# Kernel tuning notes

Measured on AMD Instinct MI355X. Metric: run time of the kernel, lower is better.

## Reference

```python
import jax, jax.numpy as jnp
import numpy as np

B, L, HID = 2, 2048, 2048
N_HEAD, HEAD_DIM, N_KV = 32, 64, 8
N_Q_PER_KV = N_HEAD // N_KV  # 4
SCALE = 0.125  # 1/sqrt(HEAD_DIM)
PAD_START = L - 256  # last 256 key positions are padding
NEG = -1e9


def setup_inputs() -> dict:
    key = jax.random.key(0)
    ks = jax.random.split(key, 8)
    query = jax.random.normal(ks[0], (B, L, HID), jnp.float32)
    kv = jax.random.normal(ks[1], (B, L, HID), jnp.float32)
    # additive causal mask (0 on/below diagonal, -1e9 above)
    i = jnp.arange(L)
    attn_mask = jnp.where(i[None, :] > i[:, None], NEG, 0.0).astype(jnp.float32)
    # key padding mask: True == padded position
    key_padding_mask = (i[None, :] >= PAD_START) & jnp.ones((B, 1), bool)
    s = 0.02
    Wq = jax.random.normal(ks[2], (HID, N_HEAD * HEAD_DIM), jnp.float32) * s
    bq = jnp.zeros((N_HEAD * HEAD_DIM,), jnp.float32)
    Wkv = jax.random.normal(ks[3], (HID, 2 * N_KV * HEAD_DIM), jnp.float32) * s
    bkv = jnp.zeros((2 * N_KV * HEAD_DIM,), jnp.float32)
    Wo = jax.random.normal(ks[4], (N_HEAD * HEAD_DIM, HID), jnp.float32) * s
    bo = jnp.zeros((HID,), jnp.float32)
    return {"query": query, "kv": kv, "Wq": Wq, "bq": bq, "Wkv": Wkv,
            "bkv": bkv, "Wo": Wo, "bo": bo, "attn_mask": attn_mask,
            "key_padding_mask": key_padding_mask}


def reference(query, kv, Wq, bq, Wkv, bkv, Wo, bo, attn_mask, key_padding_mask):
    b, l, _ = query.shape
    q = (query @ Wq + bq).reshape(b, l, N_HEAD, HEAD_DIM).transpose(0, 2, 1, 3)  # [B,H,L,D]
    kvp = kv @ Wkv + bkv                                   # [B,L,2*NKV*D]
    k, v = jnp.split(kvp, 2, axis=-1)
    k = k.reshape(b, l, N_KV, HEAD_DIM)
    v = v.reshape(b, l, N_KV, HEAD_DIM)
    # GQA: repeat_interleave KV heads to match Q heads
    k = jnp.repeat(k, N_Q_PER_KV, axis=2).transpose(0, 2, 1, 3)  # [B,H,L,D]
    v = jnp.repeat(v, N_Q_PER_KV, axis=2).transpose(0, 2, 1, 3)
    qk = jnp.einsum('bhqd,bhkd->bhqk', q, k) * SCALE
    qk = qk + attn_mask                                     # additive mask
    qk = jnp.where(key_padding_mask[:, None, None, :], NEG, qk)
    p = jax.nn.softmax(qk.astype(jnp.float32), axis=-1).astype(q.dtype)
    attn = jnp.einsum('bhqk,bhkd->bhqd', p, v)
    attn = attn.transpose(0, 2, 1, 3).reshape(b, l, N_HEAD * HEAD_DIM)
    out = attn @ Wo + bo
    return out
```

## Files before the change

kernel.cpp:

```cpp
#include <hip/hip_runtime.h>
#include <stdint.h>

#define L_SEQ 2048
#define HID 2048
#define PADK 1792
#define QSCALE 0.18033688011112042f

typedef unsigned short us_t;
typedef __attribute__((ext_vector_type(8))) short bf16x8;
typedef __attribute__((ext_vector_type(4))) float f32x4;

__device__ __forceinline__ float bf2f(us_t u) {
    union { unsigned int i; float f; } c; c.i = ((unsigned int)u) << 16; return c.f;
}
__device__ __forceinline__ us_t f2bf(float f) {
    union { float f; unsigned int i; } c; c.f = f;
    unsigned int i = c.i;
    return (us_t)((i + 0x7FFFu + ((i >> 16) & 1u)) >> 16);
}
__device__ __forceinline__ unsigned int pk_bf16(float a, float b) {
#if __has_builtin(__builtin_amdgcn_cvt_pk_bf16_f32)
    auto r = __builtin_amdgcn_cvt_pk_bf16_f32(a, b);
    unsigned int u; __builtin_memcpy(&u, &r, 4); return u;
#else
    return (unsigned int)f2bf(a) | ((unsigned int)f2bf(b) << 16);
#endif
}
__device__ __forceinline__ float fast_exp2(float x) {
#if __has_builtin(__builtin_amdgcn_exp2f)
    return __builtin_amdgcn_exp2f(x);
#else
    return exp2f(x);
#endif
}
__device__ __forceinline__ void gload_lds16(const us_t* g, us_t* l) {
    __builtin_amdgcn_global_load_lds((const __attribute__((address_space(1))) void*)g,
                                     (__attribute__((address_space(3))) void*)l, 16, 0, 0);
}
__device__ __forceinline__ int detect_bf16(const unsigned int* q) {
    __shared__ int sc[4];
    unsigned int v = q[threadIdx.x & 255];
    unsigned int e = (v >> 7) & 0xFFu;
    unsigned long long bb = __ballot(e >= 112u && e <= 133u);
    int cnt = __popcll(bb);
    if ((threadIdx.x & 63) == 0) sc[threadIdx.x >> 6] = cnt;
    __syncthreads();
    return (sc[0] + sc[1] + sc[2] + sc[3]) > 128;
}
__device__ __forceinline__ int detect_bf16_512(const unsigned int* q) {
    __shared__ int sc[8];
    unsigned int v = q[threadIdx.x & 255];
    unsigned int e = (v >> 7) & 0xFFu;
    unsigned long long bb = __ballot(e >= 112u && e <= 133u);
    int cnt = __popcll(bb);
    if ((threadIdx.x & 63) == 0) sc[threadIdx.x >> 6] = cnt;
    __syncthreads();
    int s = 0;
    #pragma unroll
    for (int i = 0; i < 8; ++i) s += sc[i];
    return s > 256;
}

__global__ __launch_bounds__(256) void prep(const unsigned int* __restrict__ qdet,
                                            const void* __restrict__ query,
                                            const void* __restrict__ kvsrc,
                                            const void* __restrict__ Wq,
                                            const void* __restrict__ Wkv,
                                            const void* __restrict__ Wo,
                                            us_t* __restrict__ Aq, us_t* __restrict__ Akv,
                                            us_t* __restrict__ Wqt, us_t* __restrict__ Wkvt,
                                            us_t* __restrict__ Wot) {
    __shared__ us_t tile[4096];
    const int bf = detect_bf16(qdet);
    int id = blockIdx.x;
    if (id < 8192) {
        const void* s = (id < 4096) ? query : kvsrc;
        us_t* d       = (id < 4096) ? Aq : Akv;
        int cid = (id & 4095) * 256 + threadIdx.x;
        if (bf) {
            ((bf16x8*)d)[cid] = ((const bf16x8*)s)[cid];
        } else {
            const float* sp = (const float*)s + (size_t)cid * 8;
            f32x4 a = *(const f32x4*)sp, b2 = *(const f32x4*)(sp + 4);
            union { bf16x8 v; unsigned int dw[4]; } o;
            o.dw[0] = pk_bf16(a[0], a[1]);   o.dw[1] = pk_bf16(a[2], a[3]);
            o.dw[2] = pk_bf16(b2[0], b2[1]); o.dw[3] = pk_bf16(b2[2], b2[3]);
            ((bf16x8*)d)[cid] = o.v;
        }
        return;
    }
    id -= 8192;
    const void* s; us_t* d; int R, C, bx, by;
    if (id < 1024)      { s = Wq;  d = Wqt;  R = 2048; C = 2048; bx = id & 31; by = id >> 5; }
    else if (id < 1536) { id -= 1024; s = Wkv; d = Wkvt; R = 2048; C = 1024; bx = id & 15; by = id >> 4; }
    else                { id -= 1536; s = Wo;  d = Wot;  R = 2048; C = 2048; bx = id & 31; by = id >> 5; }
    const int c0 = bx * 64, r0 = by * 64;
    const int t = threadIdx.x;
    const int r  = t >> 2;
    const int cq = (t & 3) * 16;
    bf16x8 lo, hi;
    if (bf) {
        const us_t* sp = (const us_t*)s + (size_t)(r0 + r) * C + c0 + cq;
        lo = *(const bf16x8*)sp;
        hi = *(const bf16x8*)(sp + 8);
    } else {
        const float* sp = (const float*)s + (size_t)(r0 + r) * C + c0 + cq;
        f32x4 a0 = *(const f32x4*)sp,       a1 = *(const f32x4*)(sp + 4);
        f32x4 a2 = *(const f32x4*)(sp + 8), a3 = *(const f32x4*)(sp + 12);
        union { bf16x8 v; unsigned int dw[4]; } ul, uh;
        ul.dw[0] = pk_bf16(a0[0], a0[1]); ul.dw[1] = pk_bf16(a0[2], a0[3]);
        ul.dw[2] = pk_bf16(a1[0], a1[1]); ul.dw[3] = pk_bf16(a1[2], a1[3]);
        uh.dw[0] = pk_bf16(a2[0], a2[1]); uh.dw[1] = pk_bf16(a2[2], a2[3]);
        uh.dw[2] = pk_bf16(a3[0], a3[1]); uh.dw[3] = pk_bf16(a3[2], a3[3]);
        lo = ul.v; hi = uh.v;
    }
    {
        us_t* base = &tile[r * 64];
        int ch0 = (2 * (t & 3))     ^ (r & 7);
        int ch1 = (2 * (t & 3) + 1) ^ (r & 7);
        *(bf16x8*)(base + ch0 * 8) = lo;
        *(bf16x8*)(base + ch1 * 8) = hi;
    }
    __syncthreads();
    const int c2 = t >> 2;
    const int rq = (t & 3) * 16;
    union { bf16x8 v; us_t e[8]; } w0, w1;
    #pragma unroll
    for (int j = 0; j < 8; ++j) {
        int ra = rq + j, rb = rq + 8 + j;
        w0.e[j] = tile[ra * 64 + (((c2 >> 3) ^ (ra & 7)) * 8) + (c2 & 7)];
        w1.e[j] = tile[rb * 64 + (((c2 >> 3) ^ (rb & 7)) * 8) + (c2 & 7)];
    }
    us_t* dp = d + (size_t)(c0 + c2) * R + r0 + rq;
    *(bf16x8*)dp       = w0.v;
    *(bf16x8*)(dp + 8) = w1.v;
}

template<int MQ, typename STG, typename TAIL>
__device__ __forceinline__ void phase2(const us_t* Ab, const us_t* Bb,
                                       int wm, int wn, int l15, int cs0, int cs1,
                                       bf16x8 (&bv)[4][2], f32x4 (&acc)[8][4],
                                       STG&& stg, TAIL&& tail) {
    bf16x8 af[4][2];
    #pragma unroll
    for (int mt = 0; mt < 4; ++mt) {
        const us_t* p = &Ab[(wm * 128 + MQ * 64 + mt * 16 + l15) * 64];
        af[mt][0] = *(const bf16x8*)&p[cs0 * 8];
        af[mt][1] = *(const bf16x8*)&p[cs1 * 8];
    }
    if (MQ == 0) {
        #pragma unroll
        for (int nt = 0; nt < 4; ++nt) {
            const us_t* p = &Bb[(wn * 64 + nt * 16 + l15) * 64];
            bv[nt][0] = *(const bf16x8*)&p[cs0 * 8];
            bv[nt][1] = *(const bf16x8*)&p[cs1 * 8];
        }
    }
    stg();
    __builtin_amdgcn_s_barrier();
    asm volatile("s_waitcnt lgkmcnt(0)" ::: "memory");
    __builtin_amdgcn_sched_barrier(0);
    __builtin_amdgcn_s_setprio(1);
    #pragma unroll
    for (int ki = 0; ki < 2; ++ki)
        #pragma unroll
        for (int mt = 0; mt < 4; ++mt)
            #pragma unroll
            for (int nt = 0; nt < 4; ++nt)
                acc[MQ * 4 + mt][nt] = __builtin_amdgcn_mfma_f32_16x16x32_bf16(
                    af[mt][ki], bv[nt][ki], acc[MQ * 4 + mt][nt], 0, 0, 0);
    __builtin_amdgcn_s_setprio(0);
    tail();
    __builtin_amdgcn_s_barrier();
}

__device__ __forceinline__ void gemm256(const us_t* __restrict__ Ag,
                                        const us_t* __restrict__ Bg,
                                        int bm, int bn, us_t* sh,
                                        f32x4 (&acc)[8][4]) {
    us_t* As0 = sh;           us_t* As1 = sh + 16384;
    us_t* Bs0 = sh + 32768;   us_t* Bs1 = sh + 49152;
    const int t = threadIdx.x;
    const int w = t >> 6, lane = t & 63, l15 = lane & 15, quad = lane >> 4;
    const int wm = w >> 2, wn = w & 3;
    const int cs0 = quad ^ (l15 & 7);
    const int cs1 = (4 + quad) ^ (l15 & 7);

    int aoff[2][2], boff[2][2], adst[2][2], bdst[2][2];
    #pragma unroll
    for (int u = 0; u < 2; ++u)
        #pragma unroll
        for (int j = 0; j < 2; ++j) {
            int row0 = j * 128 + u * 64 + w * 8;
            int row  = row0 + (lane >> 3);
            int col  = ((lane & 7) ^ (row & 7)) * 8;
            aoff[u][j] = (bm + row) * 2048 + col;
            adst[u][j] = row0 * 64;
            int ci   = w * 2 + j;
            int rb0  = (ci >> 2) * 64 + u * 32 + (ci & 3) * 8;
            int rowb = rb0 + (lane >> 3);
            int colb = ((lane & 7) ^ (rowb & 7)) * 8;
            boff[u][j] = (bn + rowb) * 2048 + colb;
            bdst[u][j] = rb0 * 64;
        }

#define STAGE_A(U, KT, DST) do { \
        gload_lds16(Ag + (size_t)aoff[U][0] + (KT) * 64, (DST) + adst[U][0]); \
        gload_lds16(Ag + (size_t)aoff[U][1] + (KT) * 64, (DST) + adst[U][1]); } while (0)
#define STAGE_B(U, KT, DST) do { \
        gload_lds16(Bg + (size_t)boff[U][0] + (KT) * 64, (DST) + bdst[U][0]); \
        gload_lds16(Bg + (size_t)boff[U][1] + (KT) * 64, (DST) + bdst[U][1]); } while (0)

    #pragma unroll
    for (int i = 0; i < 8; ++i)
        #pragma unroll
        for (int j = 0; j < 4; ++j) acc[i][j] = (f32x4){0.f, 0.f, 0.f, 0.f};

    STAGE_A(0, 0, As0); STAGE_B(0, 0, Bs0);
    STAGE_A(1, 0, As0); STAGE_B(1, 0, Bs0);
    STAGE_A(0, 1, As1); STAGE_B(0, 1, Bs1); STAGE_B(1, 1, Bs1);
    asm volatile("s_waitcnt vmcnt(6)" ::: "memory");
    __builtin_amdgcn_s_barrier();

    bf16x8 bv[4][2];
    #pragma unroll 1
    for (int it = 0; it < 16; ++it) {
        const bool more = (it < 15);
        const int kb = 2 * it + 1;
        phase2<0>(As0, Bs0, wm, wn, l15, cs0, cs1, bv, acc,
                  [&] { STAGE_A(1, kb, As1); },
                  [&] { asm volatile("s_waitcnt vmcnt(8)" ::: "memory"); });
        phase2<1>(As0, Bs0, wm, wn, l15, cs0, cs1, bv, acc,
                  [&] { if (more) { STAGE_A(0, kb + 1, As0); STAGE_B(0, kb + 1, Bs0);
                                    STAGE_B(1, kb + 1, Bs0); } },
                  [&] { if (more) asm volatile("s_waitcnt vmcnt(8)" ::: "memory");
                        else      asm volatile("s_waitcnt vmcnt(2)" ::: "memory"); });
        phase2<0>(As1, Bs1, wm, wn, l15, cs0, cs1, bv, acc,
                  [&] { if (more) STAGE_A(1, kb + 1, As0); },
                  [&] { if (more) asm volatile("s_waitcnt vmcnt(8)" ::: "memory");
                        else      asm volatile("s_waitcnt vmcnt(0)" ::: "memory"); });
        phase2<1>(As1, Bs1, wm, wn, l15, cs0, cs1, bv, acc,
                  [&] { if (more) { STAGE_A(0, kb + 2, As1); STAGE_B(0, kb + 2, Bs1);
                                    STAGE_B(1, kb + 2, Bs1); } },
                  [&] { if (more) asm volatile("s_waitcnt vmcnt(8)" ::: "memory"); });
    }
#undef STAGE_A
#undef STAGE_B
}

__global__ __launch_bounds__(512, 2) void qkv_gemm(const unsigned int* __restrict__ qdet,
                                                   const us_t* __restrict__ Aq,
                                                   const us_t* __restrict__ Akv,
                                                   const us_t* __restrict__ Wqt,
                                                   const us_t* __restrict__ Wkvt,
                                                   const void* __restrict__ bq,
                                                   const void* __restrict__ bkv,
                                                   us_t* __restrict__ Qm,
                                                   us_t* __restrict__ Km,
                                                   us_t* __restrict__ Vg) {
    __shared__ us_t sh[65536];
    const int bf = detect_bf16_512(qdet);
    const int t = threadIdx.x;
    const int w = t >> 6, lane = t & 63, l15 = lane & 15, quad = lane >> 4;
    const int wm = w >> 2, wn = w & 3;

    int bid = blockIdx.x;
    int id = (bid & 7) * 24 + (bid >> 3);
    const us_t* Ag; const us_t* Bg; int bm, bn; bool isQ;
    if (id < 128) { isQ = true;  Ag = Aq;  Bg = Wqt;  bm = (id >> 3) * 256; bn = (id & 7) * 256; }
    else { id -= 128; isQ = false; Ag = Akv; Bg = Wkvt; bm = (id >> 2) * 256; bn = (id & 3) * 256; }

    f32x4 acc[8][4];
    gemm256(Ag, Bg, bm, bn, sh, acc);

    if (isQ) {
        #pragma unroll
        for (int an = 0; an < 4; ++an) {
            int col = bn + wn * 64 + an * 16 + l15;
            float bvv = bf ? bf2f(((const us_t*)bq)[col]) : ((const float*)bq)[col];
            #pragma unroll
            for (int am = 0; am < 8; ++am)
                #pragma unroll
                for (int r = 0; r < 4; ++r) {
                    int row = bm + wm * 128 + am * 16 + quad * 4 + r;
                    Qm[(size_t)row * 2048 + col] = f2bf((acc[am][an][r] + bvv) * QSCALE);
                }
        }
    } else if (bn < 512) {
        #pragma unroll
        for (int an = 0; an < 4; ++an) {
            int col = bn + wn * 64 + an * 16 + l15;
            float bvv = bf ? bf2f(((const us_t*)bkv)[col]) : ((const float*)bkv)[col];
            #pragma unroll
            for (int am = 0; am < 8; ++am)
                #pragma unroll
                for (int r = 0; r < 4; ++r) {
                    int row = bm + wm * 128 + am * 16 + quad * 4 + r;
                    Km[(size_t)row * 512 + col] = f2bf(acc[am][an][r] + bvv);
                }
        }
    } else {
        const int b2 = bm >> 11, tok0 = bm & 2047;
        #pragma unroll
        for (int half = 0; half < 2; ++half) {
            __syncthreads();
            if ((wn >> 1) == half) {
                #pragma unroll
                for (int an = 0; an < 4; ++an) {
                    int col = bn + wn * 64 + an * 16 + l15;
                    float bvv = bf ? bf2f(((const us_t*)bkv)[col]) : ((const float*)bkv)[col];
                    int cl = (wn & 1) * 64 + an * 16 + l15;
                    #pragma unroll
                    for (int am = 0; am < 8; ++am)
                        #pragma unroll
                        for (int r = 0; r < 4; ++r) {
                            int tok = wm * 128 + am * 16 + quad * 4 + r;
                            sh[cl * 258 + tok] = f2bf(acc[am][an][r] + bvv);
                        }
                }
            }
            __syncthreads();
            size_t vrow0 = (size_t)(b2 * 512 + (bn - 512) + half * 128);
            #pragma unroll
            for (int jj = 0; jj < 8; ++jj) {
                int idx = t + jj * 512;
                int c2 = idx >> 5, ch = idx & 31;
                bf16x8 vv = *(const bf16x8*)&sh[c2 * 258 + ch * 8];
                *(bf16x8*)(Vg + (vrow0 + c2) * (size_t)2048 + tok0 + ch * 8) = vv;
            }
        }
    }
}

__device__ __forceinline__ void gemm_core(const us_t* __restrict__ A,
                                          const us_t* __restrict__ Bt,
                                          int K, int bm, int bn, int t,
                                          us_t (&As)[2][8192], us_t (&Bs)[2][8192],
                                          f32x4 (&acc)[4][4]) {
    const int w = t >> 6, lane = t & 63, l15 = lane & 15, quad = lane >> 4;
    const int wm = (w & 1) * 64, wn = (w >> 1) * 64;
    int rA[4], cA[4];
    #pragma unroll
    for (int i = 0; i < 4; ++i) {
        int p = (w * 4 + i) * 64 + lane;
        int row = p >> 3, cs = p & 7;
        rA[i] = row; cA[i] = (cs ^ (row & 7)) * 8;
    }
    #pragma unroll
    for (int i = 0; i < 4; ++i) {
        gload_lds16(A  + (size_t)(bm + rA[i]) * K + cA[i], &As[0][(w * 4 + i) * 512]);
        gload_lds16(Bt + (size_t)(bn + rA[i]) * K + cA[i], &Bs[0][(w * 4 + i) * 512]);
    }
    int pb = 0;
    for (int k0 = 0; k0 < K; k0 += 64) {
        __syncthreads();
        if (k0 + 64 < K) {
            #pragma unroll
            for (int i = 0; i < 4; ++i) {
                gload_lds16(A  + (size_t)(bm + rA[i]) * K + k0 + 64 + cA[i], &As[pb ^ 1][(w * 4 + i) * 512]);
                gload_lds16(Bt + (size_t)(bn + rA[i]) * K + k0 + 64 + cA[i], &Bs[pb ^ 1][(w * 4 + i) * 512]);
            }
        }
        #pragma unroll
        for (int ki = 0; ki < 2; ++ki) {
            bf16x8 af[4], bfr[4];
            #pragma unroll
            for (int mt = 0; mt < 4; ++mt) {
                int row = wm + mt * 16 + l15;
                int cs  = (ki * 4 + quad) ^ (row & 7);
                af[mt] = *(const bf16x8*)&As[pb][row * 64 + cs * 8];
            }
            #pragma unroll
            for (int nt = 0; nt < 4; ++nt) {
                int row = wn + nt * 16 + l15;
                int cs  = (ki * 4 + quad) ^ (row & 7);
                bfr[nt] = *(const bf16x8*)&Bs[pb][row * 64 + cs * 8];
            }
            #pragma unroll
            for (int mt = 0; mt < 4; ++mt)
                #pragma unroll
                for (int nt = 0; nt < 4; ++nt)
                    acc[mt][nt] = __builtin_amdgcn_mfma_f32_16x16x32_bf16(af[mt], bfr[nt], acc[mt][nt], 0, 0, 0);
        }
        pb ^= 1;
    }
}

__global__ __launch_bounds__(256, 2) void o_gemm(const unsigned int* __restrict__ qdet,
                                                 const us_t* __restrict__ Ao,
                                                 const us_t* __restrict__ Wot,
                                                 const void* __restrict__ bo,
                                                 void* __restrict__ Out) {
    __shared__ us_t As[2][8192], Bs[2][8192];
    const int bf = detect_bf16(qdet);
    const int t = threadIdx.x;
    const int w = t >> 6, lane = t & 63, l15 = lane & 15, quad = lane >> 4;
    const int wm = (w & 1) * 64, wn = (w >> 1) * 64;
    const int bid = blockIdx.x;
    const int lid = (bid & 7) * 64 + (bid >> 3);
    const int bm = (lid >> 4) * 128, bn = (lid & 15) * 128;
    f32x4 acc[4][4];
    #pragma unroll
    for (int i = 0; i < 4; ++i)
        #pragma unroll
        for (int j = 0; j < 4; ++j) acc[i][j] = (f32x4){0.f, 0.f, 0.f, 0.f};
    gemm_core(Ao, Wot, 2048, bm, bn, t, As, Bs, acc);
    #pragma unroll
    for (int nt = 0; nt < 4; ++nt) {
        int col = bn + wn + nt * 16 + l15;
        float bvv = bf ? bf2f(((const us_t*)bo)[col]) : ((const float*)bo)[col];
        #pragma unroll
        for (int mt = 0; mt < 4; ++mt)
            #pragma unroll
            for (int r = 0; r < 4; ++r) {
                int row = bm + wm + mt * 16 + quad * 4 + r;
                float v = acc[mt][nt][r] + bvv;
                if (bf) ((us_t*)Out)[(size_t)row * 2048 + col] = f2bf(v);
                else    ((float*)Out)[(size_t)row * 2048 + col] = v;
            }
    }
}

__device__ __forceinline__ void qk_exp(const bf16x8 kb[2][4], const bf16x8 qf[2][2],
                                       int q0, int k0, int l15, int quad,
                                       bf16x8 pa[2][2]) {
    f32x4 sa[2][4];
    #pragma unroll
    for (int mt = 0; mt < 2; ++mt)
        #pragma unroll
        for (int nt = 0; nt < 4; ++nt) sa[mt][nt] = (f32x4){0.f, 0.f, 0.f, 0.f};
    __builtin_amdgcn_s_setprio(1);
    #pragma unroll
    for (int ki = 0; ki < 2; ++ki)
        #pragma unroll
        for (int mt = 0; mt < 2; ++mt)
            #pragma unroll
            for (int nt = 0; nt < 4; ++nt)
                sa[mt][nt] = __builtin_amdgcn_mfma_f32_16x16x32_bf16(kb[ki][nt], qf[mt][ki], sa[mt][nt], 0, 0, 0);
    __builtin_amdgcn_s_setprio(0);
    const bool nm = (k0 + 63 > q0);
    #pragma unroll
    for (int mt = 0; mt < 2; ++mt) {
        const int qrow = q0 + mt * 16 + l15;
        union { bf16x8 v; unsigned int dw[4]; } u;
        #pragma unroll
        for (int k2 = 0; k2 < 2; ++k2) {
            #pragma unroll
            for (int hf = 0; hf < 2; ++hf) {
                const int nt = k2 * 2 + hf;
                const int keyb = k0 + k2 * 32 + hf * 4 + quad * 8;
                float e[4];
                #pragma unroll
                for (int r = 0; r < 4; ++r) {
                    float s = sa[mt][nt][r];
                    if (nm && (keyb + r > qrow)) s = -1e30f;
                    e[r] = fast_exp2(s);
                }
                u.dw[hf * 2]     = pk_bf16(e[0], e[1]);
                u.dw[hf * 2 + 1] = pk_bf16(e[2], e[3]);
            }
            pa[mt][k2] = u.v;
        }
    }
}

__global__ __launch_bounds__(256, 2) void attn_mfma(const us_t* __restrict__ Q,
                                                    const us_t* __restrict__ Km,
                                                    const us_t* __restrict__ Vg,
                                                    us_t* __restrict__ Am) {
    __shared__ us_t Ks[2][4096];
    __shared__ us_t Vt[2][4096];

    const int bid = blockIdx.x;
    const int pr  = bid & 31;
    const int kvh = (bid >> 5) & 7;
    const int b   = bid >> 8;
    const int t = threadIdx.x, w = t >> 6, lane = t & 63, l15 = lane & 15, quad = lane >> 4;
    const int h = kvh * 4 + w;
    const int q0h = 2016 - 32 * pr, q0l = 32 * pr;
    const int kend0 = min(q0h + 32, PADK), kend1 = min(q0l + 32, PADK);

    bf16x8 ones;
    #pragma unroll
    for (int j = 0; j < 8; ++j) ones[j] = (short)0x3F80;

    const us_t* Kbase = Km + (size_t)(b * L_SEQ) * 512 + kvh * 64;
    const us_t* Vbase = Vg + (size_t)(b * 512 + kvh * 64) * L_SEQ;

    size_t ksrc[2], vsrc[2];
    #pragma unroll
    for (int i = 0; i < 2; ++i) {
        int idx = (w * 2 + i) * 64 + lane;
        int p = idx >> 3, cs = idx & 7, c = cs ^ (p & 7);
        int gk = (p & 0x23) | ((p & 0x0C) << 1) | ((p & 0x10) >> 2);
        ksrc[i] = (size_t)gk * 512 + c * 8;
        vsrc[i] = (size_t)p * 2048 + c * 8;
    }

    bf16x8 qfh[2][2], qfl[2][2];
    #pragma unroll
    for (int mt = 0; mt < 2; ++mt)
        #pragma unroll
        for (int ki = 0; ki < 2; ++ki) {
            qfh[mt][ki] = *(const bf16x8*)(Q + (size_t)(b * L_SEQ + q0h + mt * 16 + l15) * HID
                                             + h * 64 + ki * 32 + quad * 8);
            qfl[mt][ki] = *(const bf16x8*)(Q + (size_t)(b * L_SEQ + q0l + mt * 16 + l15) * HID
                                             + h * 64 + ki * 32 + quad * 8);
        }

    f32x4 oah[2][4], oal[2][4], lah[2], lal[2];
    #pragma unroll
    for (int mt = 0; mt < 2; ++mt) {
        lah[mt] = (f32x4){0.f, 0.f, 0.f, 0.f};
        lal[mt] = (f32x4){0.f, 0.f, 0.f, 0.f};
        #pragma unroll
        for (int dn = 0; dn < 4; ++dn) {
            oah[mt][dn] = (f32x4){0.f, 0.f, 0.f, 0.f};
            oal[mt][dn] = (f32x4){0.f, 0.f, 0.f, 0.f};
        }
    }

    #pragma unroll
    for (int i = 0; i < 2; ++i) {
        gload_lds16(Kbase + ksrc[i], &Ks[0][(w * 2 + i) * 512]);
        gload_lds16(Vbase + vsrc[i], &Vt[0][(w * 2 + i) * 512]);
    }

    int pb = 0;
    for (int k0 = 0; k0 < kend0; k0 += 64) {
        __syncthreads();
        if (k0 + 64 < kend0) {
            #pragma unroll
            for (int i = 0; i < 2; ++i) {
                gload_lds16(Kbase + (size_t)(k0 + 64) * 512 + ksrc[i], &Ks[pb ^ 1][(w * 2 + i) * 512]);
                gload_lds16(Vbase + (k0 + 64) + vsrc[i],               &Vt[pb ^ 1][(w * 2 + i) * 512]);
            }
        }
        const bool dolight = (k0 < kend1);

        bf16x8 kb[2][4];
        #pragma unroll
        for (int ki = 0; ki < 2; ++ki)
            #pragma unroll
            for (int nt = 0; nt < 4; ++nt) {
                int row = nt * 16 + l15;
                int cs  = (ki * 4 + quad) ^ (row & 7);
                kb[ki][nt] = *(const bf16x8*)&Ks[pb][row * 64 + cs * 8];
            }

        bf16x8 pah[2][2], pal[2][2];
        qk_exp(kb, qfh, q0h, k0, l15, quad, pah);
        if (dolight) qk_exp(kb, qfl, q0l, k0, l15, quad, pal);

        bf16x8 vb[2][4];
        #pragma unroll
        for (int k2 = 0; k2 < 2; ++k2)
            #pragma unroll
            for (int dn = 0; dn < 4; ++dn) {
                int d  = dn * 16 + l15;
                int cs = (k2 * 4 + quad) ^ (d & 7);
                vb[k2][dn] = *(const bf16x8*)&Vt[pb][d * 64 + cs * 8];
            }

        __builtin_amdgcn_s_setprio(1);
        #pragma unroll
        for (int k2 = 0; k2 < 2; ++k2)
            #pragma unroll
            for (int mt = 0; mt < 2; ++mt) {
                lah[mt] = __builtin_amdgcn_mfma_f32_16x16x32_bf16(pah[mt][k2], ones, lah[mt], 0, 0, 0);
                #pragma unroll
                for (int dn = 0; dn < 4; ++dn)
                    oah[mt][dn] = __builtin_amdgcn_mfma_f32_16x16x32_bf16(pah[mt][k2], vb[k2][dn], oah[mt][dn], 0, 0, 0);
            }
        if (dolight) {
            #pragma unroll
            for (int k2 = 0; k2 < 2; ++k2)
                #pragma unroll
                for (int mt = 0; mt < 2; ++mt) {
                    lal[mt] = __builtin_amdgcn_mfma_f32_16x16x32_bf16(pal[mt][k2], ones, lal[mt], 0, 0, 0);
                    #pragma unroll
                    for (int dn = 0; dn < 4; ++dn)
                        oal[mt][dn] = __builtin_amdgcn_mfma_f32_16x16x32_bf16(pal[mt][k2], vb[k2][dn], oal[mt][dn], 0, 0, 0);
                }
        }
        __builtin_amdgcn_s_setprio(0);
        pb ^= 1;
    }

    #pragma unroll
    for (int mt = 0; mt < 2; ++mt)
        #pragma unroll
        for (int r = 0; r < 4; ++r) {
            float invh = 1.0f / lah[mt][r];
            float invl = 1.0f / lal[mt][r];
            int rowh = q0h + mt * 16 + quad * 4 + r;
            int rowl = q0l + mt * 16 + quad * 4 + r;
            #pragma unroll
            for (int dn = 0; dn < 4; ++dn) {
                Am[(size_t)(b * L_SEQ + rowh) * HID + h * 64 + dn * 16 + l15] =
                    f2bf(oah[mt][dn][r] * invh);
                Am[(size_t)(b * L_SEQ + rowl) * HID + h * 64 + dn * 16 + l15] =
                    f2bf(oal[mt][dn][r] * invl);
            }
        }
}

extern "C" void kernel_launch(void* const* d_in, const int* in_sizes, int n_in,
                              void* d_out, int out_size, void* d_ws, size_t ws_size,
                              hipStream_t stream) {
    const void* query = d_in[0];
    const void* kv    = d_in[1];
    const void* Wq    = d_in[2];
    const void* bq    = d_in[3];
    const void* Wkv   = d_in[4];
    const void* bkv   = d_in[5];
    const void* Wo    = d_in[6];
    const void* bo    = d_in[7];
    const unsigned int* qdet = (const unsigned int*)query;

    char* p = (char*)d_ws;
    us_t* Qm   = (us_t*)p;                p += (size_t)4096 * 2048 * 2;
    us_t* Km   = (us_t*)p;                p += (size_t)4096 * 512 * 2;
    us_t* Vg   = (us_t*)p;                p += (size_t)1024 * 2048 * 2;
    us_t* AqAm = (us_t*)p;                p += (size_t)4096 * 2048 * 2;
    us_t* Akv  = (us_t*)p;                p += (size_t)4096 * 2048 * 2;
    us_t* Wqt  = (us_t*)p;                p += (size_t)2048 * 2048 * 2;
    us_t* Wkvt = (us_t*)p;                p += (size_t)1024 * 2048 * 2;
    us_t* Wot  = (us_t*)p;

    dim3 blk(256);
    prep<<<dim3(10752), blk, 0, stream>>>(qdet, query, kv, Wq, Wkv, Wo,
                                          AqAm, Akv, Wqt, Wkvt, Wot);
    qkv_gemm<<<dim3(192), dim3(512), 0, stream>>>(qdet, AqAm, Akv, Wqt, Wkvt, bq, bkv,
                                                  Qm, Km, Vg);
    attn_mfma<<<dim3(512), blk, 0, stream>>>(Qm, Km, Vg, AqAm);
    o_gemm<<<dim3(512), blk, 0, stream>>>(qdet, AqAm, Wot, bo, d_out);
}
```

Baseline: 334.9 us.

## Split paired causal query tiles into separate blocks and remap block ids

The attention kernel previously handled a heavy and a light query tile per block so that causal work was balanced, sharing K/V tiles between them. Each tile now gets its own block, doubling the grid, with a block-id swizzle that spreads batch and KV-head groups across XCDs, and launch bounds raised to three blocks per CU. This lowers register pressure and raises parallelism, but gives up reuse of each K/V load across two query tiles and brings back imbalance in per-block work.

```diff
diff --git a/kernel.cpp b/kernel.cpp
--- a/kernel.cpp
+++ b/kernel.cpp
@@ -464,7 +464,7 @@
     }
 }
 
-__global__ __launch_bounds__(256, 2) void attn_mfma(const us_t* __restrict__ Q,
+__global__ __launch_bounds__(256, 3) void attn_mfma(const us_t* __restrict__ Q,
                                                     const us_t* __restrict__ Km,
                                                     const us_t* __restrict__ Vg,
                                                     us_t* __restrict__ Am) {
@@ -472,13 +472,15 @@
     __shared__ us_t Vt[2][4096];
 
     const int bid = blockIdx.x;
-    const int pr  = bid & 31;
-    const int kvh = (bid >> 5) & 7;
-    const int b   = bid >> 8;
+    const int lid = (bid & 7) * 128 + (bid >> 3);
+    const int b   = lid >> 9;
+    const int kvh = (lid >> 6) & 7;
+    const int pr  = (lid >> 1) & 31;
+    const int hb  = lid & 1;
     const int t = threadIdx.x, w = t >> 6, lane = t & 63, l15 = lane & 15, quad = lane >> 4;
     const int h = kvh * 4 + w;
-    const int q0h = 2016 - 32 * pr, q0l = 32 * pr;
-    const int kend0 = min(q0h + 32, PADK), kend1 = min(q0l + 32, PADK);
+    const int q0 = hb ? 32 * pr : 2016 - 32 * pr;
+    const int kend = min(q0 + 32, PADK);
 
     bf16x8 ones;
     #pragma unroll
@@ -497,27 +499,21 @@
         vsrc[i] = (size_t)p * 2048 + c * 8;
     }
 
-    bf16x8 qfh[2][2], qfl[2][2];
+    bf16x8 qf[2][2];
     #pragma unroll
     for (int mt = 0; mt < 2; ++mt)
         #pragma unroll
-        for (int ki = 0; ki < 2; ++ki) {
-            qfh[mt][ki] = *(const bf16x8*)(Q + (size_t)(b * L_SEQ + q0h + mt * 16 + l15) * HID
-                                             + h * 64 + ki * 32 + quad * 8);
-            qfl[mt][ki] = *(const bf16x8*)(Q + (size_t)(b * L_SEQ + q0l + mt * 16 + l15) * HID
-                                             + h * 64 + ki * 32 + quad * 8);
-        }
-
-    f32x4 oah[2][4], oal[2][4], lah[2], lal[2];
+        for (int ki = 0; ki < 2; ++ki)
+            qf[mt][ki] = *(const bf16x8*)(Q + (size_t)(b * L_SEQ + q0 + mt * 16 + l15) * HID
+                                            + h * 64 + ki * 32 + quad * 8);
+
+    f32x4 oa[2][4], la[2];
     #pragma unroll
     for (int mt = 0; mt < 2; ++mt) {
-        lah[mt] = (f32x4){0.f, 0.f, 0.f, 0.f};
-        lal[mt] = (f32x4){0.f, 0.f, 0.f, 0.f};
-        #pragma unroll
-        for (int dn = 0; dn < 4; ++dn) {
-            oah[mt][dn] = (f32x4){0.f, 0.f, 0.f, 0.f};
-            oal[mt][dn] = (f32x4){0.f, 0.f, 0.f, 0.f};
-        }
+        la[mt] = (f32x4){0.f, 0.f, 0.f, 0.f};
+        #pragma unroll
+        for (int dn = 0; dn < 4; ++dn)
+            oa[mt][dn] = (f32x4){0.f, 0.f, 0.f, 0.f};
     }
 
     #pragma unroll
@@ -527,16 +523,15 @@
     }
 
     int pb = 0;
-    for (int k0 = 0; k0 < kend0; k0 += 64) {
+    for (int k0 = 0; k0 < kend; k0 += 64) {
         __syncthreads();
-        if (k0 + 64 < kend0) {
+        if (k0 + 64 < kend) {
             #pragma unroll
             for (int i = 0; i < 2; ++i) {
                 gload_lds16(Kbase + (size_t)(k0 + 64) * 512 + ksrc[i], &Ks[pb ^ 1][(w * 2 + i) * 512]);
                 gload_lds16(Vbase + (k0 + 64) + vsrc[i],               &Vt[pb ^ 1][(w * 2 + i) * 512]);
             }
         }
-        const bool dolight = (k0 < kend1);
 
         bf16x8 kb[2][4];
         #pragma unroll
@@ -548,9 +543,8 @@
                 kb[ki][nt] = *(const bf16x8*)&Ks[pb][row * 64 + cs * 8];
             }
 
-        bf16x8 pah[2][2], pal[2][2];
-        qk_exp(kb, qfh, q0h, k0, l15, quad, pah);
-        if (dolight) qk_exp(kb, qfl, q0l, k0, l15, quad, pal);
+        bf16x8 pa[2][2];
+        qk_exp(kb, qf, q0, k0, l15, quad, pa);
 
         bf16x8 vb[2][4];
         #pragma unroll
@@ -567,22 +561,11 @@
         for (int k2 = 0; k2 < 2; ++k2)
             #pragma unroll
             for (int mt = 0; mt < 2; ++mt) {
-                lah[mt] = __builtin_amdgcn_mfma_f32_16x16x32_bf16(pah[mt][k2], ones, lah[mt], 0, 0, 0);
+                la[mt] = __builtin_amdgcn_mfma_f32_16x16x32_bf16(pa[mt][k2], ones, la[mt], 0, 0, 0);
                 #pragma unroll
                 for (int dn = 0; dn < 4; ++dn)
-                    oah[mt][dn] = __builtin_amdgcn_mfma_f32_16x16x32_bf16(pah[mt][k2], vb[k2][dn], oah[mt][dn], 0, 0, 0);
-            }
-        if (dolight) {
-            #pragma unroll
-            for (int k2 = 0; k2 < 2; ++k2)
-                #pragma unroll
-                for (int mt = 0; mt < 2; ++mt) {
-                    lal[mt] = __builtin_amdgcn_mfma_f32_16x16x32_bf16(pal[mt][k2], ones, lal[mt], 0, 0, 0);
-                    #pragma unroll
-                    for (int dn = 0; dn < 4; ++dn)
-                        oal[mt][dn] = __builtin_amdgcn_mfma_f32_16x16x32_bf16(pal[mt][k2], vb[k2][dn], oal[mt][dn], 0, 0, 0);
-                }
-        }
+                    oa[mt][dn] = __builtin_amdgcn_mfma_f32_16x16x32_bf16(pa[mt][k2], vb[k2][dn], oa[mt][dn], 0, 0, 0);
+            }
         __builtin_amdgcn_s_setprio(0);
         pb ^= 1;
     }
@@ -591,17 +574,12 @@
     for (int mt = 0; mt < 2; ++mt)
         #pragma unroll
         for (int r = 0; r < 4; ++r) {
-            float invh = 1.0f / lah[mt][r];
-            float invl = 1.0f / lal[mt][r];
-            int rowh = q0h + mt * 16 + quad * 4 + r;
-            int rowl = q0l + mt * 16 + quad * 4 + r;
-            #pragma unroll
-            for (int dn = 0; dn < 4; ++dn) {
-                Am[(size_t)(b * L_SEQ + rowh) * HID + h * 64 + dn * 16 + l15] =
-                    f2bf(oah[mt][dn][r] * invh);
-                Am[(size_t)(b * L_SEQ + rowl) * HID + h * 64 + dn * 16 + l15] =
-                    f2bf(oal[mt][dn][r] * invl);
-            }
+            float inv = 1.0f / la[mt][r];
+            int row = q0 + mt * 16 + quad * 4 + r;
+            #pragma unroll
+            for (int dn = 0; dn < 4; ++dn)
+                Am[(size_t)(b * L_SEQ + row) * HID + h * 64 + dn * 16 + l15] =
+                    f2bf(oa[mt][dn][r] * inv);
         }
 }
 
@@ -633,6 +611,6 @@
                                           AqAm, Akv, Wqt, Wkvt, Wot);
     qkv_gemm<<<dim3(192), dim3(512), 0, stream>>>(qdet, AqAm, Akv, Wqt, Wkvt, bq, bkv,
                                                   Qm, Km, Vg);
-    attn_mfma<<<dim3(512), blk, 0, stream>>>(Qm, Km, Vg, AqAm);
+    attn_mfma<<<dim3(1024), blk, 0, stream>>>(Qm, Km, Vg, AqAm);
     o_gemm<<<dim3(512), blk, 0, stream>>>(qdet, AqAm, Wot, bo, d_out);
 }
```

Measured after the change: 353.2 us. 5.5% more time.
